# Kernel optimization log

Measured on AMD Instinct MI355X. Metric: run time of the kernel, lower is better.

## Reference

```python
import jax, jax.numpy as jnp
import numpy as np

COMPRESSION = 2  # max-pool factor along flattened spatial axis for phi and g


def setup_inputs() -> dict:
    key = jax.random.key(0)
    ks = jax.random.split(key, 5)
    B, C, H, W = 4, 64, 96, 96
    Ci = 32  # intermediate_dim = C // 2
    s = 1.0 / np.sqrt(C)
    return {
        "x": jax.random.normal(ks[0], (B, C, H, W), dtype=jnp.float32),
        "w_theta": jax.random.normal(ks[1], (Ci, C), dtype=jnp.float32) * s,
        "b_theta": jnp.zeros((Ci,), dtype=jnp.float32),
        "w_phi": jax.random.normal(ks[2], (Ci, C), dtype=jnp.float32) * s,
        "b_phi": jnp.zeros((Ci,), dtype=jnp.float32),
        "w_g": jax.random.normal(ks[3], (Ci, C), dtype=jnp.float32) * s,
        "b_g": jnp.zeros((Ci,), dtype=jnp.float32),
        "w_out": jax.random.normal(ks[4], (C, Ci), dtype=jnp.float32) * (1.0 / np.sqrt(Ci)),
        "b_out": jnp.zeros((C,), dtype=jnp.float32),
    }


def reference(x, w_theta, b_theta, w_phi, b_phi, w_g, b_g, w_out, b_out):
    B, C, H, W = x.shape
    N = H * W
    xf = x.reshape(B, C, N).transpose(0, 2, 1)            # [B, N, C]
    # 1x1 conv projections == channel matmuls
    theta = xf @ w_theta.T + b_theta                      # [B, N, Ci]
    phi = xf @ w_phi.T + b_phi                            # [B, N, Ci]
    g = xf @ w_g.T + b_g                                  # [B, N, Ci]
    # compression: max-pool (kernel=stride=COMPRESSION) along flattened spatial axis
    Ci = theta.shape[-1]
    phi = phi.reshape(B, N // COMPRESSION, COMPRESSION, Ci).max(axis=2)  # [B, N/c, Ci]
    g = g.reshape(B, N // COMPRESSION, COMPRESSION, Ci).max(axis=2)      # [B, N/c, Ci]
    # embedded-gaussian affinity + softmax
    attn = jax.nn.softmax(jnp.einsum('bnc,bmc->bnm', theta, phi), axis=-1)  # [B, N, N/c]
    y = jnp.einsum('bnm,bmc->bnc', attn, g)               # [B, N, Ci]
    out = y @ w_out.T + b_out                             # [B, N, C]
    out = out.transpose(0, 2, 1).reshape(B, C, H, W)
    return out + x  # residual
```

## Files before the change

### kernel.cpp

```cpp
#include <hip/hip_runtime.h>
#include <hip/hip_bf16.h>


#define NQ 9216
#define MM 4608
#define TPW 18
#define LOG2E 1.44269504088896340736f

typedef __attribute__((ext_vector_type(8))) short bf16x8;
typedef __attribute__((ext_vector_type(4))) float f32x4;
typedef __attribute__((ext_vector_type(4))) unsigned short u16x4;

static __device__ __forceinline__ unsigned pk2(float a, float b) {
    __hip_bfloat162 h = __float22bfloat162_rn(make_float2(a, b));
    return *reinterpret_cast<unsigned*>(&h);
}

__global__ __launch_bounds__(128, 4) void proj_kernel(
    const float* __restrict__ x,
    const float* __restrict__ wt, const float* __restrict__ bt,
    const float* __restrict__ wp, const float* __restrict__ bp,
    const float* __restrict__ wg, const float* __restrict__ bg,
    unsigned short* __restrict__ theta, unsigned short* __restrict__ phi,
    unsigned short* __restrict__ gT)
{
    __shared__ unsigned short gst[32 * 20];

    const int tid  = threadIdx.x;
    const int wid  = tid >> 6;
    const int lane = tid & 63;
    const int q = lane >> 4;
    const int c = lane & 15;

    const int b     = blockIdx.x / 288;
    const int rem   = blockIdx.x % 288;
    const int n0    = rem * 32 + wid * 16;

    const float* Wm[3] = {wt, wp, wg};
    const float* Bm[3] = {bt, bp, bg};

    bf16x8 wf[3][2][2];
    float bias[3][2];
#pragma unroll
    for (int p = 0; p < 3; ++p) {
#pragma unroll
        for (int ct = 0; ct < 2; ++ct) {
            bias[p][ct] = Bm[p][ct * 16 + c];
#pragma unroll
            for (int ks = 0; ks < 2; ++ks) {
                const float* wsrc = Wm[p] + (ct * 16 + c) * 64 + ks * 32 + q * 8;
                f32x4 w0 = *(const f32x4*)wsrc;
                f32x4 w1 = *(const f32x4*)(wsrc + 4);
                unsigned* wk = (unsigned*)&wf[p][ct][ks];
                wk[0] = pk2(w0[0], w0[1]); wk[1] = pk2(w0[2], w0[3]);
                wk[2] = pk2(w1[0], w1[1]); wk[3] = pk2(w1[2], w1[3]);
            }
        }
    }

    bf16x8 af[2];
#pragma unroll
    for (int ks = 0; ks < 2; ++ks) {
        unsigned* ap = (unsigned*)&af[ks];
#pragma unroll
        for (int j2 = 0; j2 < 4; ++j2) {
            float x0 = x[(b * 64 + ks * 32 + q * 8 + j2 * 2) * NQ + n0 + c];
            float x1 = x[(b * 64 + ks * 32 + q * 8 + j2 * 2 + 1) * NQ + n0 + c];
            ap[j2] = pk2(x0, x1);
        }
    }

#pragma unroll
    for (int p = 0; p < 3; ++p) {
#pragma unroll
        for (int ct = 0; ct < 2; ++ct) {
            f32x4 acc = {0.f, 0.f, 0.f, 0.f};
            acc = __builtin_amdgcn_mfma_f32_16x16x32_bf16(af[0], wf[p][ct][0], acc, 0, 0, 0);
            acc = __builtin_amdgcn_mfma_f32_16x16x32_bf16(af[1], wf[p][ct][1], acc, 0, 0, 0);
#pragma unroll
            for (int r = 0; r < 4; ++r) acc[r] += bias[p][ct];
            const int ci = ct * 16 + c;
            if (p == 0) {
                unsigned pv0 = pk2(acc[0] * LOG2E, acc[1] * LOG2E);
                unsigned pv1 = pk2(acc[2] * LOG2E, acc[3] * LOG2E);
                theta[(b * NQ + n0 + 4 * q + 0) * 32 + ci] = (unsigned short)pv0;
                theta[(b * NQ + n0 + 4 * q + 1) * 32 + ci] = (unsigned short)(pv0 >> 16);
                theta[(b * NQ + n0 + 4 * q + 2) * 32 + ci] = (unsigned short)pv1;
                theta[(b * NQ + n0 + 4 * q + 3) * 32 + ci] = (unsigned short)(pv1 >> 16);
            } else {
                unsigned pv = pk2(fmaxf(acc[0], acc[1]), fmaxf(acc[2], acc[3]));
                if (p == 1) {
                    const int m0 = (n0 >> 1) + 2 * q;
                    phi[(b * MM + m0) * 32 + ci]     = (unsigned short)pv;
                    phi[(b * MM + m0 + 1) * 32 + ci] = (unsigned short)(pv >> 16);
                } else {
                    *(unsigned int*)(gst + ci * 20 + wid * 8 + 2 * q) = pv;
                }
            }
        }
    }

    __syncthreads();
    {
        const int ci = tid >> 2;
        const int m4 = (tid & 3) * 4;
        u16x4 v = *(const u16x4*)(gst + ci * 20 + m4);
        *(u16x4*)(gT + (b * 32 + ci) * MM + rem * 16 + m4) = v;
    }
}

__global__ __launch_bounds__(512, 6) void attn_kernel(
    const unsigned short* __restrict__ theta, const unsigned short* __restrict__ phi,
    const unsigned short* __restrict__ gT,
    const float* __restrict__ w_out, const float* __restrict__ b_out,
    const float* __restrict__ x, float* __restrict__ out)
{
    __shared__ union SharedU {
        unsigned short pld[8][48 * 32];
        struct {
            float red[4][48][36];
            float lred[4][48];
            unsigned short yld[32][50];
        } ep;
    } sh;

    const int tid  = threadIdx.x;
    const int w    = tid >> 6;
    const int lane = tid & 63;
    const int q  = lane >> 4;
    const int c  = lane & 15;
    const int sw = ((c >> 1) & 3) << 3;

    const int b  = blockIdx.x / 192;
    const int nb = (blockIdx.x % 192) * 48;

    bf16x8 qf[3];
#pragma unroll
    for (int rt = 0; rt < 3; ++rt)
        qf[rt] = *(const bf16x8*)(theta + (b * NQ + nb + rt * 16 + c) * 32 + q * 8);

    const unsigned short* phiB = phi + (size_t)b * MM * 32;
    const unsigned short* gTB  = gT + (size_t)b * 32 * MM;
    unsigned short* myp = sh.pld[w];

    f32x4 acc[3][2];
    float lsum[3];
#pragma unroll
    for (int rt = 0; rt < 3; ++rt) {
        lsum[rt] = 0.f;
#pragma unroll
        for (int s2 = 0; s2 < 2; ++s2) acc[rt][s2] = (f32x4){0.f, 0.f, 0.f, 0.f};
    }

    const int t0 = w * TPW;
    bf16x8 kf[2], vf[2];

#define LOAD_KF(m0) do {                                                      \
    kf[0] = *(const bf16x8*)(phiB + ((m0) + c) * 32 + q * 8);                 \
    kf[1] = *(const bf16x8*)(phiB + ((m0) + 16 + c) * 32 + q * 8);            \
} while (0)

#define LOAD_VF(m0) do {                                                      \
    vf[0] = *(const bf16x8*)(gTB + c * MM + (m0) + q * 8);                    \
    vf[1] = *(const bf16x8*)(gTB + (16 + c) * MM + (m0) + q * 8);             \
} while (0)

#define S_STEP(rt) do {                                                      \
    _Pragma("unroll")                                                        \
    for (int mct = 0; mct < 2; ++mct) {                                      \
        f32x4 z = {0.f, 0.f, 0.f, 0.f};                                      \
        f32x4 s = __builtin_amdgcn_mfma_f32_16x16x32_bf16(kf[mct], qf[rt], z, 0, 0, 0); \
        float e0 = __builtin_amdgcn_exp2f(s[0]);                             \
        float e1 = __builtin_amdgcn_exp2f(s[1]);                             \
        float e2 = __builtin_amdgcn_exp2f(s[2]);                             \
        float e3 = __builtin_amdgcn_exp2f(s[3]);                             \
        lsum[rt] += (e0 + e1) + (e2 + e3);                                   \
        uint2 hv = {pk2(e0, e1), pk2(e2, e3)};                               \
        *(uint2*)(myp + (((rt) * 16 + c) << 5) + ((mct * 16 + 4 * q) ^ sw)) = hv; \
    }                                                                        \
} while (0)

#define PV_STEP(rt) do {                                                     \
    bf16x8 pf = *(const bf16x8*)(myp + (((rt) * 16 + c) << 5) + ((q * 8) ^ sw)); \
    acc[rt][0] = __builtin_amdgcn_mfma_f32_16x16x32_bf16(vf[0], pf, acc[rt][0], 0, 0, 0); \
    acc[rt][1] = __builtin_amdgcn_mfma_f32_16x16x32_bf16(vf[1], pf, acc[rt][1], 0, 0, 0); \
} while (0)

    LOAD_KF(t0 * 32);
    LOAD_VF(t0 * 32);
    S_STEP(0); S_STEP(1); S_STEP(2);

    for (int mi = 1; mi < TPW; ++mi) {
        const int m0 = (t0 + mi) * 32;
        LOAD_KF(m0);
        PV_STEP(0); PV_STEP(1); PV_STEP(2);
        LOAD_VF(m0);
        S_STEP(0); S_STEP(1); S_STEP(2);
    }

    PV_STEP(0); PV_STEP(1); PV_STEP(2);

#undef LOAD_KF
#undef LOAD_VF
#undef S_STEP
#undef PV_STEP

    float lv[3];
#pragma unroll
    for (int rt = 0; rt < 3; ++rt) {
        float v = lsum[rt];
        v += __shfl_xor(v, 16);
        v += __shfl_xor(v, 32);
        lv[rt] = v;
    }

    __syncthreads();

    if (w < 4) {
        if (lane < 16) {
            sh.ep.lred[w][lane]      = lv[0];
            sh.ep.lred[w][16 + lane] = lv[1];
            sh.ep.lred[w][32 + lane] = lv[2];
        }
#pragma unroll
        for (int rt = 0; rt < 3; ++rt)
#pragma unroll
            for (int s2 = 0; s2 < 2; ++s2)
                *(f32x4*)&sh.ep.red[w][rt * 16 + c][s2 * 16 + 4 * q] = acc[rt][s2];
    }
    __syncthreads();

    if (w >= 4) {
        const int tw = w - 4;
        if (lane < 16) {
            sh.ep.lred[tw][lane]      += lv[0];
            sh.ep.lred[tw][16 + lane] += lv[1];
            sh.ep.lred[tw][32 + lane] += lv[2];
        }
#pragma unroll
        for (int rt = 0; rt < 3; ++rt)
#pragma unroll
            for (int s2 = 0; s2 < 2; ++s2) {
                float* p = &sh.ep.red[tw][rt * 16 + c][s2 * 16 + 4 * q];
                f32x4 cur = *(f32x4*)p;
                *(f32x4*)p = cur + acc[rt][s2];
            }
    }
    __syncthreads();

    if (tid < 384) {
        const int n  = tid % 48;
        const int cg = (tid / 48) * 4;
        float ls = (sh.ep.lred[0][n] + sh.ep.lred[1][n]) +
                   (sh.ep.lred[2][n] + sh.ep.lred[3][n]);
        float inv = 1.0f / ls;
        f32x4 s = {0.f, 0.f, 0.f, 0.f};
#pragma unroll
        for (int ww = 0; ww < 4; ++ww)
            s += *(const f32x4*)&sh.ep.red[ww][n][cg];
#pragma unroll
        for (int k = 0; k < 4; ++k)
            sh.ep.yld[cg + k][n] = (unsigned short)(pk2(s[k] * inv, 0.f) & 0xffff);
    }
    __syncthreads();

    if (w < 4) {
        bf16x8 wof;
        {
            const float* wsrc = w_out + (w * 16 + c) * 32 + q * 8;
            f32x4 w0 = *(const f32x4*)wsrc;
            f32x4 w1 = *(const f32x4*)(wsrc + 4);
            unsigned* wk = (unsigned*)&wof;
            wk[0] = pk2(w0[0], w0[1]); wk[1] = pk2(w0[2], w0[3]);
            wk[2] = pk2(w1[0], w1[1]); wk[3] = pk2(w1[2], w1[3]);
        }
#pragma unroll
        for (int nt = 0; nt < 3; ++nt) {
            bf16x8 yf;
            unsigned short* yp = (unsigned short*)&yf;
#pragma unroll
            for (int j = 0; j < 8; ++j)
                yp[j] = sh.ep.yld[q * 8 + j][nt * 16 + c];
            f32x4 z = {0.f, 0.f, 0.f, 0.f};
            f32x4 o = __builtin_amdgcn_mfma_f32_16x16x32_bf16(wof, yf, z, 0, 0, 0);
#pragma unroll
            for (int r = 0; r < 4; ++r) {
                const int chn = w * 16 + 4 * q + r;
                const size_t addr = (size_t)(b * 64 + chn) * NQ + nb + nt * 16 + c;
                out[addr] = o[r] + b_out[chn] + x[addr];
            }
        }
    }
}

extern "C" void kernel_launch(void* const* d_in, const int* in_sizes, int n_in,
                              void* d_out, int out_size, void* d_ws, size_t ws_size,
                              hipStream_t stream) {
    const float* x       = (const float*)d_in[0];
    const float* w_theta = (const float*)d_in[1];
    const float* b_theta = (const float*)d_in[2];
    const float* w_phi   = (const float*)d_in[3];
    const float* b_phi   = (const float*)d_in[4];
    const float* w_g     = (const float*)d_in[5];
    const float* b_g     = (const float*)d_in[6];
    const float* w_out   = (const float*)d_in[7];
    const float* b_out   = (const float*)d_in[8];
    float* out = (float*)d_out;

    unsigned short* theta = (unsigned short*)d_ws;
    unsigned short* phi   = theta + 4 * NQ * 32;
    unsigned short* gT    = phi + 4 * MM * 32;

    proj_kernel<<<1152, 128, 0, stream>>>(x, w_theta, b_theta, w_phi, b_phi,
                                          w_g, b_g, theta, phi, gT);
    attn_kernel<<<768, 512, 0, stream>>>(theta, phi, gT, w_out, b_out, x, out);
}
```

Measured before the change: 146.5 us.

## Halve attention block to 4 waves, each covering twice the key range

The attention kernel now runs 256 threads (4 waves) per block instead of 8, and each wave processes 36 key tiles rather than 18. This removes the two-stage cross-wave partial-sum reduction in the epilogue and one barrier, and shrinks the P staging buffer in shared memory. In exchange there is less parallelism per query block and a longer serial loop per wave, with only 768 blocks to hide latency.

```diff
diff --git a/kernel.cpp b/kernel.cpp
--- a/kernel.cpp
+++ b/kernel.cpp
@@ -4,7 +4,7 @@
 
 #define NQ 9216
 #define MM 4608
-#define TPW 18
+#define TPW 36
 #define LOG2E 1.44269504088896340736f
 
 typedef __attribute__((ext_vector_type(8))) short bf16x8;
@@ -109,14 +109,14 @@
     }
 }
 
-__global__ __launch_bounds__(512, 6) void attn_kernel(
+__global__ __launch_bounds__(256, 4) void attn_kernel(
     const unsigned short* __restrict__ theta, const unsigned short* __restrict__ phi,
     const unsigned short* __restrict__ gT,
     const float* __restrict__ w_out, const float* __restrict__ b_out,
     const float* __restrict__ x, float* __restrict__ out)
 {
     __shared__ union SharedU {
-        unsigned short pld[8][48 * 32];
+        unsigned short pld[4][48 * 32];
         struct {
             float red[4][48][36];
             float lred[4][48];
@@ -216,55 +216,40 @@
 
     __syncthreads();
 
-    if (w < 4) {
-        if (lane < 16) {
-            sh.ep.lred[w][lane]      = lv[0];
-            sh.ep.lred[w][16 + lane] = lv[1];
-            sh.ep.lred[w][32 + lane] = lv[2];
-        }
-#pragma unroll
-        for (int rt = 0; rt < 3; ++rt)
-#pragma unroll
-            for (int s2 = 0; s2 < 2; ++s2)
-                *(f32x4*)&sh.ep.red[w][rt * 16 + c][s2 * 16 + 4 * q] = acc[rt][s2];
-    }
+    if (lane < 16) {
+        sh.ep.lred[w][lane]      = lv[0];
+        sh.ep.lred[w][16 + lane] = lv[1];
+        sh.ep.lred[w][32 + lane] = lv[2];
+    }
+#pragma unroll
+    for (int rt = 0; rt < 3; ++rt)
+#pragma unroll
+        for (int s2 = 0; s2 < 2; ++s2)
+            *(f32x4*)&sh.ep.red[w][rt * 16 + c][s2 * 16 + 4 * q] = acc[rt][s2];
+
     __syncthreads();
 
-    if (w >= 4) {
-        const int tw = w - 4;
-        if (lane < 16) {
-            sh.ep.lred[tw][lane]      += lv[0];
-            sh.ep.lred[tw][16 + lane] += lv[1];
-            sh.ep.lred[tw][32 + lane] += lv[2];
-        }
-#pragma unroll
-        for (int rt = 0; rt < 3; ++rt)
-#pragma unroll
-            for (int s2 = 0; s2 < 2; ++s2) {
-                float* p = &sh.ep.red[tw][rt * 16 + c][s2 * 16 + 4 * q];
-                f32x4 cur = *(f32x4*)p;
-                *(f32x4*)p = cur + acc[rt][s2];
-            }
-    }
-    __syncthreads();
-
-    if (tid < 384) {
-        const int n  = tid % 48;
-        const int cg = (tid / 48) * 4;
+    if (tid < 192) {
+        const int n   = tid % 48;
+        const int cig = (tid / 48) * 8;
         float ls = (sh.ep.lred[0][n] + sh.ep.lred[1][n]) +
                    (sh.ep.lred[2][n] + sh.ep.lred[3][n]);
         float inv = 1.0f / ls;
-        f32x4 s = {0.f, 0.f, 0.f, 0.f};
-#pragma unroll
-        for (int ww = 0; ww < 4; ++ww)
-            s += *(const f32x4*)&sh.ep.red[ww][n][cg];
-#pragma unroll
-        for (int k = 0; k < 4; ++k)
-            sh.ep.yld[cg + k][n] = (unsigned short)(pk2(s[k] * inv, 0.f) & 0xffff);
+        f32x4 s0 = {0.f, 0.f, 0.f, 0.f}, s1 = {0.f, 0.f, 0.f, 0.f};
+#pragma unroll
+        for (int ww = 0; ww < 4; ++ww) {
+            s0 += *(const f32x4*)&sh.ep.red[ww][n][cig];
+            s1 += *(const f32x4*)&sh.ep.red[ww][n][cig + 4];
+        }
+#pragma unroll
+        for (int k = 0; k < 4; ++k) {
+            sh.ep.yld[cig + k][n]     = (unsigned short)(pk2(s0[k] * inv, 0.f) & 0xffff);
+            sh.ep.yld[cig + 4 + k][n] = (unsigned short)(pk2(s1[k] * inv, 0.f) & 0xffff);
+        }
     }
     __syncthreads();
 
-    if (w < 4) {
+    {
         bf16x8 wof;
         {
             const float* wsrc = w_out + (w * 16 + c) * 32 + q * 8;
@@ -313,5 +298,5 @@
 
     proj_kernel<<<1152, 128, 0, stream>>>(x, w_theta, b_theta, w_phi, b_phi,
                                           w_g, b_g, theta, phi, gT);
-    attn_kernel<<<768, 512, 0, stream>>>(theta, phi, gT, w_out, b_out, x, out);
+    attn_kernel<<<768, 256, 0, stream>>>(theta, phi, gT, w_out, b_out, x, out);
 }
```

Result: faster. 129.4 us (-11.7%).
